# Kernel optimization log

Measured on AMD Instinct MI355X. Metric: run time of the kernel, lower is better.

## Reference

```python
import jax, jax.numpy as jnp
import numpy as np

EPS = 1e-5
ABIT = 8
WBIT = 8


def ste_round(x):
    # straight-through rounding (HAWQ SymmetricQuantFunction)
    return x + jax.lax.stop_gradient(jnp.round(x) - x)


def quant_act(x, bit=ABIT):
    # per-tensor symmetric activation quantization (QuantAct)
    n = 2.0 ** (bit - 1) - 1  # 127
    scale = jnp.max(jnp.abs(x)) / n
    x_int = jnp.clip(ste_round(x / scale), -n - 1, n)
    return x_int * scale, scale


def setup_inputs() -> dict:
    key = jax.random.key(0)
    k = jax.random.split(key, 6)
    B, C_in, H, W, C_out = 32, 512, 32, 32, 128
    x = jax.random.normal(k[0], (B, C_in, H, W), jnp.float32)
    # incoming activation scale (input assumed already 8-bit quantized)
    act_scaling_factor = (jnp.max(jnp.abs(x)) / 127.0).reshape(1)
    bn_gamma = jax.random.uniform(k[1], (C_in,), jnp.float32, 0.5, 1.5)
    bn_beta = jax.random.normal(k[2], (C_in,), jnp.float32) * 0.1
    bn_mean = jax.random.normal(k[3], (C_in,), jnp.float32) * 0.1
    bn_var = jax.random.uniform(k[4], (C_in,), jnp.float32, 0.5, 1.5)
    conv_weight = jax.random.normal(k[5], (C_out, C_in, 3, 3), jnp.float32) / np.sqrt(C_in * 9)
    return {"x": x, "act_scaling_factor": act_scaling_factor,
            "bn_gamma": bn_gamma, "bn_beta": bn_beta,
            "bn_mean": bn_mean, "bn_var": bn_var,
            "conv_weight": conv_weight}


def reference(x, act_scaling_factor, bn_gamma, bn_beta, bn_mean, bn_var, conv_weight):
    nw = 2.0 ** (WBIT - 1) - 1  # 127
    s_in = act_scaling_factor.reshape(())

    # ---- QuantBn: fold BN into per-channel affine, quantize weight/bias ----
    w_bn = bn_gamma / jnp.sqrt(bn_var + EPS)            # [C_in]
    b_bn = bn_beta - bn_mean * w_bn                      # [C_in]
    ws_bn = jnp.max(jnp.abs(w_bn)) / nw                  # per-tensor weight scale
    w_int = jnp.clip(ste_round(w_bn / ws_bn), -nw - 1, nw)
    bn_sf = ws_bn * s_in                                 # bn output scaling factor
    b_int = ste_round(b_bn / bn_sf)
    x_int = x / s_in
    x = (x_int * w_int[None, :, None, None] + b_int[None, :, None, None]) * bn_sf

    # ---- ReLU ----
    x = jax.nn.relu(x)

    # ---- QuantAct: requantize activations to 8 bit ----
    x, s_act = quant_act(x)

    # ---- QuantConv2d: per-output-channel 8-bit weight quant, int conv ----
    ws_c = jnp.max(jnp.abs(conv_weight), axis=(1, 2, 3)) / nw       # [C_out]
    w_cint = jnp.clip(ste_round(conv_weight / ws_c[:, None, None, None]), -nw - 1, nw)
    y_int = jax.lax.conv_general_dilated(
        x / s_act, w_cint, window_strides=(1, 1), padding=((1, 1), (1, 1)),
        dimension_numbers=("NCHW", "OIHW", "NCHW"))
    conv_sf = s_act * ws_c                               # [C_out]
    y = y_int * conv_sf[None, :, None, None]

    # ---- QuantAct output requant ----
    y, s_out = quant_act(y)
    return (y, s_out)
```

## Files before the change

### kernel.cpp

```cpp
#include <hip/hip_runtime.h>


typedef int v4i __attribute__((ext_vector_type(4)));

#define WS_A1    64
#define WS_B1    2176
#define WS_WSC   4224
#define WS_XMX   4736
#define WS_XMN   6784
#define WS_WQ    12288
#define WS_X2    602112
#define WS_ZROW  18427904

__device__ __forceinline__ float wave_max(float m) {
#pragma unroll
    for (int off = 32; off; off >>= 1) m = fmaxf(m, __shfl_xor(m, off));
    return m;
}

__global__ __launch_bounds__(512) void k_prep(
    const float* __restrict__ gamma, const float* __restrict__ beta,
    const float* __restrict__ mean,  const float* __restrict__ var,
    const float* __restrict__ asf,   const float* __restrict__ cw,
    const float4* __restrict__ x4,
    float* ws_f, unsigned* ws_u, float* __restrict__ wsc,
    signed char* __restrict__ wq) {
    int t = threadIdx.x;
    int bid = blockIdx.x;
    __shared__ float red[16];
    if (bid < 128) {
        int co = bid;
        const float* w = cw + (size_t)co * 4608;
        float m = 0.f;
        for (int j = t; j < 4608; j += 512) m = fmaxf(m, fabsf(w[j]));
        m = wave_max(m);
        if ((t & 63) == 0) red[t >> 6] = m;
        __syncthreads();
        float mall = red[0];
#pragma unroll
        for (int i = 1; i < 8; ++i) mall = fmaxf(mall, red[i]);
        float sc = mall / 127.0f;
        if (t == 0) wsc[co] = sc;
#pragma unroll
        for (int tap = 0; tap < 9; ++tap) {
            float q = fminf(fmaxf(rintf(w[t * 9 + tap] / sc), -128.f), 127.f);
            wq[(((size_t)(tap * 8 + (t >> 6)) * 128 + co) * 64) + (t & 63)] = (signed char)q;
        }
    } else if (bid == 128) {
        float wbn = gamma[t] / sqrtf(var[t] + 1e-5f);
        float bbn = beta[t] - mean[t] * wbn;
        float m = wave_max(fabsf(wbn));
        if ((t & 63) == 0) red[t >> 6] = m;
        __syncthreads();
        float mall = red[0];
#pragma unroll
        for (int i = 1; i < 8; ++i) mall = fmaxf(mall, red[i]);
        float ws_bn = mall / 127.0f;
        float s_in  = asf[0];
        float bn_sf = ws_bn * s_in;
        float wint  = fminf(fmaxf(rintf(wbn / ws_bn), -128.f), 127.f);
        float bint  = rintf(bbn / bn_sf);
        ws_f[WS_A1 / 4 + t] = wint * bn_sf / s_in;
        ws_f[WS_B1 / 4 + t] = bint * bn_sf;
        if (t == 0) ws_u[1] = 0u;
    } else {
        int c = bid - 129;
        float mx = -3.4e38f, mn = 3.4e38f;
#pragma unroll
        for (int r = 0; r < 16; ++r) {
            int bbb = r * 2 + (t >> 8);
            float4 v = x4[((size_t)(bbb * 512 + c)) * 256 + (t & 255)];
            mx = fmaxf(mx, fmaxf(fmaxf(v.x, v.y), fmaxf(v.z, v.w)));
            mn = fminf(mn, fminf(fminf(v.x, v.y), fminf(v.z, v.w)));
        }
        mx = wave_max(mx);
        mn = -wave_max(-mn);
        if ((t & 63) == 0) { red[t >> 6] = mx; red[8 + (t >> 6)] = mn; }
        __syncthreads();
        if (t == 0) {
            float M = red[0], N = red[8];
#pragma unroll
            for (int i = 1; i < 8; ++i) { M = fmaxf(M, red[i]); N = fminf(N, red[8 + i]); }
            ws_f[WS_XMX / 4 + c] = M;
            ws_f[WS_XMN / 4 + c] = N;
        }
    }
}

__global__ __launch_bounds__(256) void k_xquant(
    const float4* __restrict__ x4, float* __restrict__ ws_f,
    unsigned* __restrict__ x2u, unsigned* __restrict__ zrowu) {
    int bb = blockIdx.x >> 5, h = blockIdx.x & 31;
    const float* A1 = ws_f + WS_A1 / 4;
    const float* B1 = ws_f + WS_B1 / 4;
    const float* XMX = ws_f + WS_XMX / 4;
    const float* XMN = ws_f + WS_XMN / 4;
    int t = threadIdx.x;

    __shared__ float sred[4];
    float cand = 0.f;
#pragma unroll
    for (int c0 = 0; c0 < 512; c0 += 256) {
        int c = c0 + t;
        float A = A1[c], B = B1[c];
        cand = fmaxf(cand, fmaxf(fmaf(XMX[c], A, B), fmaf(XMN[c], A, B)));
    }
    cand = wave_max(cand);
    if ((t & 63) == 0) sred[t >> 6] = cand;
    __syncthreads();
    float xm = fmaxf(fmaxf(sred[0], sred[1]), fmaxf(sred[2], sred[3]));
    float inv_sact = 127.0f / xm;
    if (blockIdx.x == 0 && t == 0) ws_f[3] = xm / 127.0f;

    {
        int cc = t >> 5, rem = t & 31;
        int wp = (rem >> 4) * 33, inner = rem & 15;
        x2u[((size_t)(((bb * 32 + h) * 8 + cc) * 34 + wp)) * 16 + inner] = 0u;
    }
    if (blockIdx.x < 17) {
        int idx = blockIdx.x * 256 + t;
        if (idx < 4352) zrowu[idx] = 0u;
    }

    __shared__ unsigned lds[512 * 9];

#pragma unroll
    for (int it = 0; it < 16; ++it) {
        int idx = it * 256 + t;
        int c = idx >> 3, f4 = idx & 7;
        float4 v = x4[((size_t)bb * 512 + c) * 256 + h * 8 + f4];
        float A = A1[c] * inv_sact, B = B1[c] * inv_sact;
        unsigned q0 = (unsigned)(int)fminf(rintf(fmaxf(fmaf(v.x, A, B), 0.f)), 127.f);
        unsigned q1 = (unsigned)(int)fminf(rintf(fmaxf(fmaf(v.y, A, B), 0.f)), 127.f);
        unsigned q2 = (unsigned)(int)fminf(rintf(fmaxf(fmaf(v.z, A, B), 0.f)), 127.f);
        unsigned q3 = (unsigned)(int)fminf(rintf(fmaxf(fmaf(v.w, A, B), 0.f)), 127.f);
        lds[c * 9 + f4] = q0 | (q1 << 8) | (q2 << 16) | (q3 << 24);
    }
    __syncthreads();

#pragma unroll
    for (int it2 = 0; it2 < 4; ++it2) {
        int cdw = (t & 31) + ((t >> 6) << 5);
        int wq4 = ((t >> 5) & 1) + (it2 << 1);
        unsigned u0 = lds[(4 * cdw + 0) * 9 + wq4];
        unsigned u1 = lds[(4 * cdw + 1) * 9 + wq4];
        unsigned u2 = lds[(4 * cdw + 2) * 9 + wq4];
        unsigned u3 = lds[(4 * cdw + 3) * 9 + wq4];
        int cc = cdw >> 4, inner = cdw & 15;
        unsigned* dst = x2u + ((size_t)(((bb * 32 + h) * 8 + cc) * 34 + wq4 * 4 + 1)) * 16 + inner;
#pragma unroll
        for (int k = 0; k < 4; ++k) {
            unsigned o = ((u0 >> (8 * k)) & 255) | (((u1 >> (8 * k)) & 255) << 8) |
                         (((u2 >> (8 * k)) & 255) << 16) | (((u3 >> (8 * k)) & 255) << 24);
            dst[(size_t)k * 16] = o;
        }
    }
}

__global__ __launch_bounds__(256, 3) void k_conv(
    const unsigned char* __restrict__ x2, const unsigned char* __restrict__ zrow,
    const signed char* __restrict__ wq,
    const float* __restrict__ wsc, const float* __restrict__ ws_f,
    unsigned* __restrict__ amaxy, float* __restrict__ y) {
    __shared__ v4i red[3][1024];
    int t = threadIdx.x;
    int lane = t & 63, kv = t >> 6;
    int m = lane & 15, quad = lane >> 4;

    int bid = blockIdx.x;
    int tile = (bid & 7) * 128 + (bid >> 3);
    int ch = tile & 1;
    int rowpair = (tile >> 1) & 15;
    int bb = tile >> 5;
    int h0 = rowpair * 2;
    int co0 = ch * 64;

    const unsigned char* xb = x2 + (size_t)bb * (32 * 8 * 34 * 64);
    const unsigned char* rp[4];
#pragma unroll
    for (int j = 0; j < 4; ++j) {
        int row = h0 - 1 + j;
        rp[j] = ((unsigned)row < 32u) ? (xb + (size_t)row * (8 * 34 * 64)) : zrow;
    }

    v4i acc[4][4];
#pragma unroll
    for (int i = 0; i < 4; ++i)
#pragma unroll
        for (int j = 0; j < 4; ++j) acc[i][j] = (v4i){0, 0, 0, 0};

    const v4i* pwv = (const v4i*)wq + (co0 + m) * 4 + quad;

#pragma unroll
    for (int kh = 0; kh < 3; ++kh)
#pragma unroll
        for (int kw = 0; kw < 3; ++kw) {
            int tap = kh * 3 + kw;
#pragma unroll
            for (int cc = 0; cc < 2; ++cc) {
                int ci = kv * 2 + cc;
                v4i a[4];
#pragma unroll
                for (int mt = 0; mt < 4; ++mt)
                    a[mt] = *((const v4i*)rp[kh + (mt >> 1)] +
                              (ci * 34 + m + (mt & 1) * 16 + kw) * 4 + quad);
#pragma unroll
                for (int nt = 0; nt < 4; ++nt) {
                    v4i bf = pwv[tap * 4096 + ci * 512 + nt * 64];
#pragma unroll
                    for (int mt = 0; mt < 4; ++mt)
                        acc[mt][nt] = __builtin_amdgcn_mfma_i32_16x16x64_i8(a[mt], bf, acc[mt][nt], 0, 0, 0);
                }
            }
        }

    if (kv > 0) {
#pragma unroll
        for (int mt = 0; mt < 4; ++mt)
#pragma unroll
            for (int nt = 0; nt < 4; ++nt)
                red[kv - 1][(mt * 4 + nt) * 64 + lane] = acc[mt][nt];
    }
    __syncthreads();
    if (kv == 0) {
#pragma unroll
        for (int r = 0; r < 3; ++r)
#pragma unroll
            for (int mt = 0; mt < 4; ++mt)
#pragma unroll
                for (int nt = 0; nt < 4; ++nt) {
                    v4i p = red[r][(mt * 4 + nt) * 64 + lane];
                    acc[mt][nt].x += p.x; acc[mt][nt].y += p.y;
                    acc[mt][nt].z += p.z; acc[mt][nt].w += p.w;
                }

        float s_act = ws_f[3];
        float mx = 0.f;
#pragma unroll
        for (int nt = 0; nt < 4; ++nt) {
            int co = co0 + nt * 16 + m;
            float sf = s_act * wsc[co];
#pragma unroll
            for (int mt = 0; mt < 4; ++mt) {
                int row = h0 + (mt >> 1);
                float* yb = y + ((size_t)(bb * 128 + co)) * 1024 + row * 32 + (mt & 1) * 16;
                float4 vv;
                vv.x = (float)acc[mt][nt][0] * sf;
                vv.y = (float)acc[mt][nt][1] * sf;
                vv.z = (float)acc[mt][nt][2] * sf;
                vv.w = (float)acc[mt][nt][3] * sf;
                *(float4*)(yb + quad * 4) = vv;
                mx = fmaxf(mx, fmaxf(fmaxf(fabsf(vv.x), fabsf(vv.y)),
                                     fmaxf(fabsf(vv.z), fabsf(vv.w))));
            }
        }
        mx = wave_max(mx);
        if (lane == 0) atomicMax(amaxy, __float_as_uint(mx));
    }
}

__global__ __launch_bounds__(256) void k_yquant(float* __restrict__ yout,
                                                const unsigned* __restrict__ ws_u) {
    float s_out = __uint_as_float(ws_u[1]) / 127.0f;
    float4* y4 = (float4*)yout;
    int stride = gridDim.x * blockDim.x;
    for (int i = blockIdx.x * blockDim.x + threadIdx.x; i < 1048576; i += stride) {
        float4 v = y4[i];
        v.x = fminf(fmaxf(rintf(v.x / s_out), -128.f), 127.f) * s_out;
        v.y = fminf(fmaxf(rintf(v.y / s_out), -128.f), 127.f) * s_out;
        v.z = fminf(fmaxf(rintf(v.z / s_out), -128.f), 127.f) * s_out;
        v.w = fminf(fmaxf(rintf(v.w / s_out), -128.f), 127.f) * s_out;
        y4[i] = v;
    }
    if (blockIdx.x == 0 && threadIdx.x == 0) yout[4194304] = s_out;
}

extern "C" void kernel_launch(void* const* d_in, const int* in_sizes, int n_in,
                              void* d_out, int out_size, void* d_ws, size_t ws_size,
                              hipStream_t stream) {
    const float* x     = (const float*)d_in[0];
    const float* asf   = (const float*)d_in[1];
    const float* gamma = (const float*)d_in[2];
    const float* beta  = (const float*)d_in[3];
    const float* mean  = (const float*)d_in[4];
    const float* var   = (const float*)d_in[5];
    const float* cw    = (const float*)d_in[6];

    float*    ws_f = (float*)d_ws;
    unsigned* ws_u = (unsigned*)d_ws;
    signed char*   wq   = (signed char*)d_ws + WS_WQ;
    unsigned char* x2   = (unsigned char*)d_ws + WS_X2;
    unsigned char* zrow = (unsigned char*)d_ws + WS_ZROW;
    float* y = (float*)d_out;

    k_prep<<<641, 512, 0, stream>>>(gamma, beta, mean, var, asf, cw,
                                    (const float4*)x, ws_f, ws_u,
                                    ws_f + WS_WSC / 4, wq);
    k_xquant<<<1024, 256, 0, stream>>>((const float4*)x, ws_f,
                                       (unsigned*)x2, (unsigned*)zrow);
    k_conv<<<1024, 256, 0, stream>>>(x2, zrow, wq, ws_f + WS_WSC / 4,
                                     ws_f, ws_u + 1, y);
    k_yquant<<<1024, 256, 0, stream>>>(y, ws_u);
}
```

Baseline: 176.5 us.

## Relayout int8 activations and weights, split min/max scan, tree-reduce conv partials

Changes the packed int8 activation and weight layouts so each MFMA fragment load reads contiguous 16-byte chunks, and rewrites the transpose in k_xquant to emit uint4 stores. It also splits the per-channel min/max scan over twice as many blocks, combining the halves with order-preserving atomicMax encodings, which needs an added memset. The k-split reduction in the conv becomes a two-level tree with less LDS. The aim is better coalescing and more parallelism in the prep stage, at the cost of an extra memset launch and additional barriers in the conv epilogue.

```diff
diff --git a/kernel.cpp b/kernel.cpp
--- a/kernel.cpp
+++ b/kernel.cpp
@@ -4,18 +4,25 @@
 typedef int v4i __attribute__((ext_vector_type(4)));
 
 #define WS_A1    64
-#define WS_B1    2176
-#define WS_WSC   4224
-#define WS_XMX   4736
-#define WS_XMN   6784
-#define WS_WQ    12288
-#define WS_X2    602112
-#define WS_ZROW  18427904
+#define WS_B1    2112
+#define WS_WSC   4160
+#define WS_XMX   4672
+#define WS_XMN   6720
+#define WS_WQ    8768
+#define WS_X2    598592
+#define WS_ZROW  18424384
 
 __device__ __forceinline__ float wave_max(float m) {
 #pragma unroll
     for (int off = 32; off; off >>= 1) m = fmaxf(m, __shfl_xor(m, off));
     return m;
+}
+__device__ __forceinline__ unsigned fenc(float f) {
+    unsigned u = __float_as_uint(f);
+    return ((int)u < 0) ? ~u : (u | 0x80000000u);
+}
+__device__ __forceinline__ float fdec(unsigned k) {
+    return __uint_as_float((k & 0x80000000u) ? (k & 0x7fffffffu) : ~k);
 }
 
 __global__ __launch_bounds__(512) void k_prep(
@@ -41,10 +48,11 @@
         for (int i = 1; i < 8; ++i) mall = fmaxf(mall, red[i]);
         float sc = mall / 127.0f;
         if (t == 0) wsc[co] = sc;
+        int ci = t >> 6, cq = (t >> 4) & 3, cb = t & 15;
 #pragma unroll
         for (int tap = 0; tap < 9; ++tap) {
             float q = fminf(fmaxf(rintf(w[t * 9 + tap] / sc), -128.f), 127.f);
-            wq[(((size_t)(tap * 8 + (t >> 6)) * 128 + co) * 64) + (t & 63)] = (signed char)q;
+            wq[(((size_t)(tap * 8 + ci) * 4 + cq) * 128 + co) * 16 + cb] = (signed char)q;
         }
     } else if (bid == 128) {
         float wbn = gamma[t] / sqrtf(var[t] + 1e-5f);
@@ -64,11 +72,12 @@
         ws_f[WS_B1 / 4 + t] = bint * bn_sf;
         if (t == 0) ws_u[1] = 0u;
     } else {
-        int c = bid - 129;
+        int idx = bid - 129;
+        int c = idx >> 1, half = idx & 1;
         float mx = -3.4e38f, mn = 3.4e38f;
 #pragma unroll
-        for (int r = 0; r < 16; ++r) {
-            int bbb = r * 2 + (t >> 8);
+        for (int r = 0; r < 8; ++r) {
+            int bbb = half * 16 + r * 2 + (t >> 8);
             float4 v = x4[((size_t)(bbb * 512 + c)) * 256 + (t & 255)];
             mx = fmaxf(mx, fmaxf(fmaxf(v.x, v.y), fmaxf(v.z, v.w)));
             mn = fminf(mn, fminf(fminf(v.x, v.y), fminf(v.z, v.w)));
@@ -81,20 +90,21 @@
             float M = red[0], N = red[8];
 #pragma unroll
             for (int i = 1; i < 8; ++i) { M = fmaxf(M, red[i]); N = fminf(N, red[8 + i]); }
-            ws_f[WS_XMX / 4 + c] = M;
-            ws_f[WS_XMN / 4 + c] = N;
+            atomicMax(ws_u + WS_XMX / 4 + c, fenc(M));
+            atomicMax(ws_u + WS_XMN / 4 + c, fenc(-N));
         }
     }
 }
 
 __global__ __launch_bounds__(256) void k_xquant(
     const float4* __restrict__ x4, float* __restrict__ ws_f,
+    const unsigned* __restrict__ ws_u,
     unsigned* __restrict__ x2u, unsigned* __restrict__ zrowu) {
     int bb = blockIdx.x >> 5, h = blockIdx.x & 31;
     const float* A1 = ws_f + WS_A1 / 4;
     const float* B1 = ws_f + WS_B1 / 4;
-    const float* XMX = ws_f + WS_XMX / 4;
-    const float* XMN = ws_f + WS_XMN / 4;
+    const unsigned* XMX = ws_u + WS_XMX / 4;
+    const unsigned* XMN = ws_u + WS_XMN / 4;
     int t = threadIdx.x;
 
     __shared__ float sred[4];
@@ -103,7 +113,8 @@
     for (int c0 = 0; c0 < 512; c0 += 256) {
         int c = c0 + t;
         float A = A1[c], B = B1[c];
-        cand = fmaxf(cand, fmaxf(fmaf(XMX[c], A, B), fmaf(XMN[c], A, B)));
+        float mx = fdec(XMX[c]), mn = -fdec(XMN[c]);
+        cand = fmaxf(cand, fmaxf(fmaf(mx, A, B), fmaf(mn, A, B)));
     }
     cand = wave_max(cand);
     if ((t & 63) == 0) sred[t >> 6] = cand;
@@ -112,10 +123,10 @@
     float inv_sact = 127.0f / xm;
     if (blockIdx.x == 0 && t == 0) ws_f[3] = xm / 127.0f;
 
+    size_t rowd = (size_t)(bb * 32 + h) * 4352;
     {
-        int cc = t >> 5, rem = t & 31;
-        int wp = (rem >> 4) * 33, inner = rem & 15;
-        x2u[((size_t)(((bb * 32 + h) * 8 + cc) * 34 + wp)) * 16 + inner] = 0u;
+        int p = t >> 3, side = (t >> 2) & 1, d = t & 3;
+        x2u[rowd + (p * 34 + side * 33) * 4 + d] = 0u;
     }
     if (blockIdx.x < 17) {
         int idx = blockIdx.x * 256 + t;
@@ -139,21 +150,22 @@
     __syncthreads();
 
 #pragma unroll
-    for (int it2 = 0; it2 < 4; ++it2) {
-        int cdw = (t & 31) + ((t >> 6) << 5);
-        int wq4 = ((t >> 5) & 1) + (it2 << 1);
-        unsigned u0 = lds[(4 * cdw + 0) * 9 + wq4];
-        unsigned u1 = lds[(4 * cdw + 1) * 9 + wq4];
-        unsigned u2 = lds[(4 * cdw + 2) * 9 + wq4];
-        unsigned u3 = lds[(4 * cdw + 3) * 9 + wq4];
-        int cc = cdw >> 4, inner = cdw & 15;
-        unsigned* dst = x2u + ((size_t)(((bb * 32 + h) * 8 + cc) * 34 + wq4 * 4 + 1)) * 16 + inner;
-#pragma unroll
-        for (int k = 0; k < 4; ++k) {
-            unsigned o = ((u0 >> (8 * k)) & 255) | (((u1 >> (8 * k)) & 255) << 8) |
-                         (((u2 >> (8 * k)) & 255) << 16) | (((u3 >> (8 * k)) & 255) << 24);
-            dst[(size_t)k * 16] = o;
-        }
+    for (int it = 0; it < 4; ++it) {
+        int p = it * 8 + (t >> 5);
+        int s = (t >> 2) & 7;
+        int k = t & 3;
+        unsigned L[16];
+#pragma unroll
+        for (int j = 0; j < 16; ++j) L[j] = lds[(p * 16 + j) * 9 + s];
+        uint4 o;
+        unsigned* op = (unsigned*)&o;
+#pragma unroll
+        for (int d = 0; d < 4; ++d)
+            op[d] = ((L[4 * d] >> (8 * k)) & 255u) |
+                    (((L[4 * d + 1] >> (8 * k)) & 255u) << 8) |
+                    (((L[4 * d + 2] >> (8 * k)) & 255u) << 16) |
+                    (((L[4 * d + 3] >> (8 * k)) & 255u) << 24);
+        *(uint4*)(x2u + rowd + (size_t)(p * 34 + s * 4 + 1 + k) * 4) = o;
     }
 }
 
@@ -162,7 +174,7 @@
     const signed char* __restrict__ wq,
     const float* __restrict__ wsc, const float* __restrict__ ws_f,
     unsigned* __restrict__ amaxy, float* __restrict__ y) {
-    __shared__ v4i red[3][1024];
+    __shared__ v4i red[2][1024];
     int t = threadIdx.x;
     int lane = t & 63, kv = t >> 6;
     int m = lane & 15, quad = lane >> 4;
@@ -175,12 +187,12 @@
     int h0 = rowpair * 2;
     int co0 = ch * 64;
 
-    const unsigned char* xb = x2 + (size_t)bb * (32 * 8 * 34 * 64);
-    const unsigned char* rp[4];
+    const unsigned char* xb = x2 + (size_t)bb * (32 * 17408);
+    const v4i* rp[4];
 #pragma unroll
     for (int j = 0; j < 4; ++j) {
         int row = h0 - 1 + j;
-        rp[j] = ((unsigned)row < 32u) ? (xb + (size_t)row * (8 * 34 * 64)) : zrow;
+        rp[j] = (const v4i*)(((unsigned)row < 32u) ? (xb + (size_t)row * 17408) : zrow);
     }
 
     v4i acc[4][4];
@@ -189,7 +201,8 @@
 #pragma unroll
         for (int j = 0; j < 4; ++j) acc[i][j] = (v4i){0, 0, 0, 0};
 
-    const v4i* pwv = (const v4i*)wq + (co0 + m) * 4 + quad;
+    const v4i* pw = (const v4i*)wq + quad * 128 + co0 + m;
+    int abase = quad * 34 + m;
 
 #pragma unroll
     for (int kh = 0; kh < 3; ++kh)
@@ -202,11 +215,10 @@
                 v4i a[4];
 #pragma unroll
                 for (int mt = 0; mt < 4; ++mt)
-                    a[mt] = *((const v4i*)rp[kh + (mt >> 1)] +
-                              (ci * 34 + m + (mt & 1) * 16 + kw) * 4 + quad);
+                    a[mt] = rp[kh + (mt >> 1)][ci * 136 + abase + kw + (mt & 1) * 16];
 #pragma unroll
                 for (int nt = 0; nt < 4; ++nt) {
-                    v4i bf = pwv[tap * 4096 + ci * 512 + nt * 64];
+                    v4i bf = pw[(tap * 8 + ci) * 512 + nt * 16];
 #pragma unroll
                     for (int mt = 0; mt < 4; ++mt)
                         acc[mt][nt] = __builtin_amdgcn_mfma_i32_16x16x64_i8(a[mt], bf, acc[mt][nt], 0, 0, 0);
@@ -214,25 +226,42 @@
             }
         }
 
-    if (kv > 0) {
+    if (kv >= 2) {
 #pragma unroll
         for (int mt = 0; mt < 4; ++mt)
 #pragma unroll
             for (int nt = 0; nt < 4; ++nt)
-                red[kv - 1][(mt * 4 + nt) * 64 + lane] = acc[mt][nt];
+                red[kv - 2][(mt * 4 + nt) * 64 + lane] = acc[mt][nt];
+    }
+    __syncthreads();
+    if (kv < 2) {
+#pragma unroll
+        for (int mt = 0; mt < 4; ++mt)
+#pragma unroll
+            for (int nt = 0; nt < 4; ++nt) {
+                v4i p = red[kv][(mt * 4 + nt) * 64 + lane];
+                acc[mt][nt].x += p.x; acc[mt][nt].y += p.y;
+                acc[mt][nt].z += p.z; acc[mt][nt].w += p.w;
+            }
+    }
+    __syncthreads();
+    if (kv == 1) {
+#pragma unroll
+        for (int mt = 0; mt < 4; ++mt)
+#pragma unroll
+            for (int nt = 0; nt < 4; ++nt)
+                red[0][(mt * 4 + nt) * 64 + lane] = acc[mt][nt];
     }
     __syncthreads();
     if (kv == 0) {
 #pragma unroll
-        for (int r = 0; r < 3; ++r)
-#pragma unroll
-            for (int mt = 0; mt < 4; ++mt)
-#pragma unroll
-                for (int nt = 0; nt < 4; ++nt) {
-                    v4i p = red[r][(mt * 4 + nt) * 64 + lane];
-                    acc[mt][nt].x += p.x; acc[mt][nt].y += p.y;
-                    acc[mt][nt].z += p.z; acc[mt][nt].w += p.w;
-                }
+        for (int mt = 0; mt < 4; ++mt)
+#pragma unroll
+            for (int nt = 0; nt < 4; ++nt) {
+                v4i p = red[0][(mt * 4 + nt) * 64 + lane];
+                acc[mt][nt].x += p.x; acc[mt][nt].y += p.y;
+                acc[mt][nt].z += p.z; acc[mt][nt].w += p.w;
+            }
 
         float s_act = ws_f[3];
         float mx = 0.f;
@@ -293,10 +322,12 @@
     unsigned char* zrow = (unsigned char*)d_ws + WS_ZROW;
     float* y = (float*)d_out;
 
-    k_prep<<<641, 512, 0, stream>>>(gamma, beta, mean, var, asf, cw,
-                                    (const float4*)x, ws_f, ws_u,
-                                    ws_f + WS_WSC / 4, wq);
-    k_xquant<<<1024, 256, 0, stream>>>((const float4*)x, ws_f,
+    hipMemsetAsync((char*)d_ws + WS_XMX, 0, 4096, stream);
+
+    k_prep<<<1153, 512, 0, stream>>>(gamma, beta, mean, var, asf, cw,
+                                     (const float4*)x, ws_f, ws_u,
+                                     ws_f + WS_WSC / 4, wq);
+    k_xquant<<<1024, 256, 0, stream>>>((const float4*)x, ws_f, ws_u,
                                        (unsigned*)x2, (unsigned*)zrow);
     k_conv<<<1024, 256, 0, stream>>>(x2, zrow, wq, ws_f + WS_WSC / 4,
                                      ws_f, ws_u + 1, y);
```

Result: faster. 166.6 us (-5.6%).
